# Kernel tuning notes

Hardware: AMD Instinct MI355X
Metric: run time of the kernel (lower is better)

Reference implementation:

```python
import jax, jax.numpy as jnp
import numpy as np
from jax import lax

TOP_K = 200
IOU_THR = 0.5
SCORE_FLOOR = 0.01  # torch code breaks when top score < 0.01

BATCH, N_ANCHOR, N_CLASS_FG = 32, 24564, 80  # last dim of x = 4 + 1 + 80 = 85


def setup_inputs() -> dict:
    key = jax.random.key(0)
    k1, k2 = jax.random.split(key)
    x = jax.random.normal(k1, (BATCH, N_ANCHOR, 4 + 1 + N_CLASS_FG), dtype=jnp.float32)
    # anchors: (cx, cy, w, h) in normalized coords
    anchor = jax.random.uniform(k2, (N_ANCHOR, 4), dtype=jnp.float32, minval=0.05, maxval=0.95)
    return {"x": x, "anchor": anchor}


def _iou_one_vs_all(box1, boxes):
    # box1: [4] (x1,y1,x2,y2); boxes: [N,4] -> ious [N]
    b1x1, b1y1, b1x2, b1y2 = box1[0], box1[1], box1[2], box1[3]
    b2x1, b2y1, b2x2, b2y2 = boxes[:, 0], boxes[:, 1], boxes[:, 2], boxes[:, 3]
    area1 = (b1x2 - b1x1) * (b1y2 - b1y1)
    area2 = (b2x2 - b2x1) * (b2y2 - b2y1)
    xl = jnp.maximum(b1x1, b2x1)
    xr = jnp.minimum(b1x2, b2x2)
    yt = jnp.maximum(b1y1, b2y1)
    yb = jnp.minimum(b1y2, b2y2)
    # torch code clamps intersection extents to [0, 1]
    common = jnp.clip(xr - xl, 0.0, 1.0) * jnp.clip(yb - yt, 0.0, 1.0)
    return common / (area1 + area2 - common)


def _nms_single(cls_i, score_i, box_i):
    # cls_i [N] int, score_i [N], box_i [N,4] -> keep [TOP_K, 6]
    order = jnp.argsort(-score_i)  # descending
    c = cls_i[order].astype(box_i.dtype)
    s = score_i[order]
    b = box_i[order]
    dets = jnp.concatenate([c[:, None], s[:, None], b], axis=1)  # [N, 6]
    valid0 = jnp.ones((dets.shape[0],), dtype=bool)

    def step(valid, _):
        idx = jnp.argmax(valid)  # first still-valid (highest-score) box
        ok = valid[idx] & (s[idx] >= SCORE_FLOOR)
        row = jnp.where(ok, dets[idx], jnp.zeros((6,), dets.dtype))
        ious = _iou_one_vs_all(b[idx], b)  # [N]
        new_valid = valid & (ious < IOU_THR)
        new_valid = new_valid.at[idx].set(False)
        valid = jnp.where(ok, new_valid, valid)
        return valid, row

    _, keep = lax.scan(step, valid0, None, length=TOP_K)
    return keep  # [TOP_K, 6] = (class, score, x1, y1, x2, y2)


def _postprocess(x, anchor):
    # decode boxes
    d = x[:, :, :4]                          # [B, A, 4]
    ax, ay, aw, ah = (anchor[None, :, i] for i in range(4))  # each [1, A]
    cx = d[:, :, 0] * aw / 10.0 + ax
    cy = d[:, :, 1] * ah / 10.0 + ay
    w = jnp.exp(d[:, :, 2] / 5.0) * aw
    h = jnp.exp(d[:, :, 3] / 5.0) * ah
    box = jnp.stack([cx - w / 2.0, cy - h / 2.0, cx + w / 2.0, cy + h / 2.0], axis=2)  # [B,A,4] x1y1x2y2
    # class scores: softmax over (bg + fg), then max over foreground classes
    probs = jax.nn.softmax(x[:, :, 4:], axis=2)
    fg = probs[:, :, 1:]
    score = jnp.max(fg, axis=2)              # [B, A]
    cls = jnp.argmax(fg, axis=2)             # [B, A] foreground class index
    return jax.vmap(_nms_single)(cls, score, box)  # [B, TOP_K, 6]


def reference(x, anchor):
    return _postprocess(x, anchor)
```

## Files before the change

### kernel.cpp

```cpp
#include <hip/hip_runtime.h>
#include <math.h>

#define NB   32
#define NA   24564
#define NTOT (NB * NA)
#define NCH  85
#define TOPK 200
#define IOU_THR_F     0.5f
#define SCORE_FLOOR_F 0.01f

#define DEC_T 128
#define NMS_T 512
#define SLOTS ((NA + NMS_T - 1) / NMS_T)
#define KPASS 8
#define NPOOL (2 * NMS_T)
#define CKADDR(e) ((((e) & 15) << 6) | ((e) >> 4))

__global__ __launch_bounds__(DEC_T) void decode_kernel(
    const float* __restrict__ x, const float* __restrict__ anchor,
    float4* __restrict__ boxes, float* __restrict__ scores,
    float* __restrict__ clsf)
{
    __shared__ float tile[DEC_T * NCH];

    const int base = blockIdx.x * DEC_T;
    const float4* src = (const float4*)(x + (size_t)base * NCH);
    float4* dst = (float4*)tile;
    for (int k = threadIdx.x; k < DEC_T * NCH / 4; k += DEC_T) dst[k] = src[k];
    __syncthreads();

    const int g = base + threadIdx.x;
    const int i = g % NA;
    const float* row = tile + threadIdx.x * NCH;

    float ax = anchor[i * 4 + 0];
    float ay = anchor[i * 4 + 1];
    float aw = anchor[i * 4 + 2];
    float ah = anchor[i * 4 + 3];

    float d0 = row[0], d1 = row[1], d2 = row[2], d3 = row[3];
    float cx = __fadd_rn(__fdiv_rn(__fmul_rn(d0, aw), 10.0f), ax);
    float cy = __fadd_rn(__fdiv_rn(__fmul_rn(d1, ah), 10.0f), ay);
    float w = __fmul_rn((float)exp((double)__fdiv_rn(d2, 5.0f)), aw);
    float h = __fmul_rn((float)exp((double)__fdiv_rn(d3, 5.0f)), ah);
    float hw = __fmul_rn(w, 0.5f);
    float hh = __fmul_rn(h, 0.5f);
    boxes[g] = make_float4(__fsub_rn(cx, hw), __fsub_rn(cy, hh),
                           __fadd_rn(cx, hw), __fadd_rn(cy, hh));

    const float* z = row + 4;
    float m = z[0];
    #pragma unroll 9
    for (int k = 1; k < 81; k++) m = fmaxf(m, z[k]);

    double S = 0.0;
    double be = 0.0;
    float  bz = -INFINITY;
    int    bj = 0;
    for (int k = 0; k < 81; k++) {
        float zk = z[k];
        double e = exp((double)__fsub_rn(zk, m));
        S += e;
        if (k >= 1 && zk > bz) { bz = zk; be = e; bj = k - 1; }
    }
    scores[g] = (float)(be / S);
    clsf[g]   = (float)bj;
}

__device__ __forceinline__ bool suppressed_by(const float4 v, const float a2,
                                              const float4 w, const float a1)
{
    float xl = fmaxf(w.x, v.x);
    float xr = fminf(w.z, v.z);
    float yt = fmaxf(w.y, v.y);
    float yb = fminf(w.w, v.w);
    float cw  = fminf(fmaxf(__fsub_rn(xr, xl), 0.0f), 1.0f);
    float chh = fminf(fmaxf(__fsub_rn(yb, yt), 0.0f), 1.0f);
    float common = __fmul_rn(cw, chh);
    float denom  = __fsub_rn(__fadd_rn(a1, a2), common);
    float iou    = __fdiv_rn(common, denom);
    return !(iou < IOU_THR_F);
}

__global__ __launch_bounds__(NMS_T, 1) void nms_kernel(
    const float4* __restrict__ boxes, const float* __restrict__ scores,
    const float* __restrict__ clsf, float* __restrict__ out)
{
    __shared__ float s_score[NA];
    __shared__ unsigned long long s_ckey[NPOOL];
    __shared__ float4 s_cbox[NPOOL];

    const int b    = blockIdx.x;
    const int tid  = threadIdx.x;
    const int lane = tid & 63;
    const float*  sc = scores + (size_t)b * NA;
    const float4* bx = boxes  + (size_t)b * NA;
    const float*  cf = clsf   + (size_t)b * NA;
    float* ob = out + (size_t)b * TOPK * 6;

    float4 box[SLOTS];
    unsigned long long alive = 0ULL;
    #pragma unroll
    for (int s = 0; s < SLOTS; s++) {
        int j = tid + s * NMS_T;
        box[s] = make_float4(0.0f, 0.0f, 0.0f, 0.0f);
        if (j < NA) { box[s] = bx[j]; alive |= (1ULL << s); }
    }
    for (int j = tid; j < NA; j += NMS_T) s_score[j] = sc[j];

    float4 wbox[KPASS]; float warea[KPASS]; float wscore[KPASS]; int wj[KPASS];
    int t = 0; bool gdone = false; int npass = 0;

    {
        unsigned long long k1 = 0ULL, k2 = 0ULL; int j1 = -1, j2 = -1;
        #pragma unroll
        for (int s = 0; s < SLOTS; s++) {
            if (!(alive & (1ULL << s))) continue;
            int j = tid + s * NMS_T;
            unsigned long long kk =
                ((unsigned long long)__float_as_uint(s_score[j]) << 32) |
                ((unsigned long long)(unsigned)(NA - j) << 10);
            if (kk > k1)      { k2 = k1; j2 = j1; k1 = kk; j1 = j; }
            else if (kk > k2) { k2 = kk; j2 = j; }
        }
        int e0 = 2 * tid, e1 = 2 * tid + 1;
        s_ckey[CKADDR(e0)] = (j1 >= 0) ? (k1 | (unsigned long long)e0) : 1ULL;
        s_ckey[CKADDR(e1)] = (j2 >= 0) ? (k2 | (unsigned long long)e1) : 1ULL;
        if (j1 >= 0) s_cbox[e0] = bx[j1];
        if (j2 >= 0) s_cbox[e1] = bx[j2];
    }
    __syncthreads();

    while (true) {
        unsigned long long ck[16];
        #pragma unroll
        for (int i = 0; i < 16; i++) ck[i] = s_ckey[(i << 6) | lane];

        npass = 0;
        unsigned long long hbound = 0ULL;
        int kmax = TOPK - t; if (kmax > KPASS) kmax = KPASS;
        while (true) {
            unsigned long long lm = 0ULL;
            #pragma unroll
            for (int i = 0; i < 16; i++) if (ck[i] > lm) lm = ck[i];
            #pragma unroll
            for (int off = 32; off > 0; off >>= 1) {
                unsigned long long o = __shfl_xor(lm, off, 64);
                if (o > lm) lm = o;
            }
            if (!(lm > hbound)) break;
            float ms = __uint_as_float((unsigned)(lm >> 32));
            if (!(ms >= SCORE_FLOOR_F)) { gdone = true; break; }

            int e  = (int)(lm & 1023ULL);
            int jw = NA - (int)((lm >> 10) & 0x7FFFULL);
            float4 cb = s_cbox[e];
            float  ca = __fmul_rn(__fsub_rn(cb.z, cb.x), __fsub_rn(cb.w, cb.y));

            bool kill = false;
            #pragma unroll
            for (int k = 0; k < KPASS; k++)
                if (k < npass)
                    kill |= suppressed_by(cb, ca, wbox[k], warea[k]);

            {
                int olane = e >> 4, oi = e & 15;
                unsigned long long pk = 0ULL;
                #pragma unroll
                for (int i = 0; i < 16; i++) if (i == (oi ^ 1)) pk = ck[i];
                unsigned long long hb_c =
                    (lane == olane && pk == 0ULL) ? lm : 0ULL;
                unsigned long long hb = __shfl(hb_c, olane, 64);
                if (hb > hbound) hbound = hb;
                #pragma unroll
                for (int i = 0; i < 16; i++)
                    if (lane == olane && i == oi) ck[i] = 0ULL;
            }

            if (!kill) {
                #pragma unroll
                for (int k = 0; k < KPASS; k++)
                    if (k == npass) {
                        wbox[k] = cb; warea[k] = ca; wscore[k] = ms; wj[k] = jw;
                    }
                npass++;
                if (npass == kmax) break;
            }
        }

        #pragma unroll
        for (int k = 0; k < KPASS; k++) {
            if (k < npass && tid == (wj[k] & (NMS_T - 1))) {
                float* o6 = ob + (size_t)(t + k) * 6;
                o6[0] = cf[wj[k]];
                o6[1] = wscore[k];
                o6[2] = wbox[k].x; o6[3] = wbox[k].y;
                o6[4] = wbox[k].z; o6[5] = wbox[k].w;
            }
        }
        t += npass;
        if (gdone || t >= TOPK) break;

        __syncthreads();

        #pragma unroll
        for (int k = 0; k < KPASS; k++)
            if (k < npass && tid == (wj[k] & (NMS_T - 1)))
                alive &= ~(1ULL << (wj[k] >> 9));

        {
            unsigned long long k1 = 0ULL, k2 = 0ULL; int j1 = -1, j2 = -1;
            #pragma unroll
            for (int s = 0; s < SLOTS; s++) {
                if (!(alive & (1ULL << s))) continue;
                float4 v = box[s];
                float a2 = __fmul_rn(__fsub_rn(v.z, v.x), __fsub_rn(v.w, v.y));
                bool dead = false;
                #pragma unroll
                for (int k = 0; k < KPASS; k++)
                    if (k < npass)
                        dead |= suppressed_by(v, a2, wbox[k], warea[k]);
                if (dead) { alive &= ~(1ULL << s); continue; }
                int j = tid + s * NMS_T;
                unsigned long long kk =
                    ((unsigned long long)__float_as_uint(s_score[j]) << 32) |
                    ((unsigned long long)(unsigned)(NA - j) << 10);
                if (kk > k1)      { k2 = k1; j2 = j1; k1 = kk; j1 = j; }
                else if (kk > k2) { k2 = kk; j2 = j; }
            }
            int e0 = 2 * tid, e1 = 2 * tid + 1;
            s_ckey[CKADDR(e0)] = (j1 >= 0) ? (k1 | (unsigned long long)e0) : 1ULL;
            s_ckey[CKADDR(e1)] = (j2 >= 0) ? (k2 | (unsigned long long)e1) : 1ULL;
            if (j1 >= 0) s_cbox[e0] = bx[j1];
            if (j2 >= 0) s_cbox[e1] = bx[j2];
        }
        __syncthreads();
    }

    for (int k = t * 6 + tid; k < TOPK * 6; k += NMS_T) ob[k] = 0.0f;
}

extern "C" void kernel_launch(void* const* d_in, const int* in_sizes, int n_in,
                              void* d_out, int out_size, void* d_ws, size_t ws_size,
                              hipStream_t stream) {
    const float* x      = (const float*)d_in[0];
    const float* anchor = (const float*)d_in[1];
    float* out = (float*)d_out;

    char* ws = (char*)d_ws;
    const size_t boxes_bytes  = (size_t)NTOT * 16;
    const size_t scores_off   = (boxes_bytes + 255) & ~255ULL;
    const size_t scores_bytes = (size_t)NTOT * 4;
    const size_t cls_off      = (scores_off + scores_bytes + 255) & ~255ULL;

    float4* boxes  = (float4*)ws;
    float*  scores = (float*)(ws + scores_off);
    float*  clsf   = (float*)(ws + cls_off);

    decode_kernel<<<NTOT / DEC_T, DEC_T, 0, stream>>>(x, anchor, boxes, scores, clsf);
    nms_kernel<<<NB, NMS_T, 0, stream>>>(boxes, scores, clsf, out);
}
```

Before: 2.026 ms.

## Split candidate keys to 32-bit, use DPP wave max, move winners to LDS

Replaces the 64-bit packed candidate keys with separate 32-bit score and low-key arrays. The wave-wide max is now two 32-bit DPP reductions plus readlane instead of 64-bit shuffle-xor loops. The per-pass winner boxes move from per-thread register arrays into shared memory, and the suppression sweep is restructured into a winner-outer loop. This cuts shuffle cost and register pressure, but adds LDS reads and a second reduction per selection step.

```diff
diff --git a/kernel.cpp b/kernel.cpp
--- a/kernel.cpp
+++ b/kernel.cpp
@@ -82,13 +82,34 @@
     return !(iou < IOU_THR_F);
 }
 
+__device__ __forceinline__ unsigned wave_umax_dpp(unsigned v)
+{
+    int x = (int)v;
+    #define DPP_ST(C) { \
+        int y_ = __builtin_amdgcn_update_dpp(x, x, C, 0xF, 0xF, false); \
+        x = ((unsigned)y_ > (unsigned)x) ? y_ : x; }
+    DPP_ST(0x111)
+    DPP_ST(0x112)
+    DPP_ST(0x114)
+    DPP_ST(0x118)
+    DPP_ST(0x142)
+    DPP_ST(0x143)
+    #undef DPP_ST
+    return (unsigned)__builtin_amdgcn_readlane(x, 63);
+}
+
 __global__ __launch_bounds__(NMS_T, 1) void nms_kernel(
     const float4* __restrict__ boxes, const float* __restrict__ scores,
     const float* __restrict__ clsf, float* __restrict__ out)
 {
     __shared__ float s_score[NA];
-    __shared__ unsigned long long s_ckey[NPOOL];
+    __shared__ unsigned s_cs[NPOOL];
+    __shared__ unsigned s_cl[NPOOL];
     __shared__ float4 s_cbox[NPOOL];
+    __shared__ float4 s_pwbox[KPASS];
+    __shared__ float  s_pwarea[KPASS];
+    __shared__ float  s_pwscore[KPASS];
+    __shared__ int    s_pwj[KPASS];
 
     const int b    = blockIdx.x;
     const int tid  = threadIdx.x;
@@ -108,8 +129,7 @@
     }
     for (int j = tid; j < NA; j += NMS_T) s_score[j] = sc[j];
 
-    float4 wbox[KPASS]; float warea[KPASS]; float wscore[KPASS]; int wj[KPASS];
-    int t = 0; bool gdone = false; int npass = 0;
+    int t = 0; bool gdone = false;
 
     {
         unsigned long long k1 = 0ULL, k2 = 0ULL; int j1 = -1, j2 = -1;
@@ -124,78 +144,83 @@
             else if (kk > k2) { k2 = kk; j2 = j; }
         }
         int e0 = 2 * tid, e1 = 2 * tid + 1;
-        s_ckey[CKADDR(e0)] = (j1 >= 0) ? (k1 | (unsigned long long)e0) : 1ULL;
-        s_ckey[CKADDR(e1)] = (j2 >= 0) ? (k2 | (unsigned long long)e1) : 1ULL;
+        s_cs[CKADDR(e0)] = (j1 >= 0) ? (unsigned)(k1 >> 32) : 1u;
+        s_cl[CKADDR(e0)] = (unsigned)k1 | (unsigned)e0;
+        s_cs[CKADDR(e1)] = (j2 >= 0) ? (unsigned)(k2 >> 32) : 1u;
+        s_cl[CKADDR(e1)] = (unsigned)k2 | (unsigned)e1;
         if (j1 >= 0) s_cbox[e0] = bx[j1];
         if (j2 >= 0) s_cbox[e1] = bx[j2];
     }
     __syncthreads();
 
     while (true) {
-        unsigned long long ck[16];
+        unsigned cs[16], cl[16];
         #pragma unroll
-        for (int i = 0; i < 16; i++) ck[i] = s_ckey[(i << 6) | lane];
-
-        npass = 0;
+        for (int i = 0; i < 16; i++) {
+            cs[i] = s_cs[(i << 6) | lane];
+            cl[i] = s_cl[(i << 6) | lane];
+        }
+
+        int npass = 0;
         unsigned long long hbound = 0ULL;
         int kmax = TOPK - t; if (kmax > KPASS) kmax = KPASS;
         while (true) {
-            unsigned long long lm = 0ULL;
-            #pragma unroll
-            for (int i = 0; i < 16; i++) if (ck[i] > lm) lm = ck[i];
-            #pragma unroll
-            for (int off = 32; off > 0; off >>= 1) {
-                unsigned long long o = __shfl_xor(lm, off, 64);
-                if (o > lm) lm = o;
-            }
+            unsigned msl = 0u;
+            #pragma unroll
+            for (int i = 0; i < 16; i++) msl = (cs[i] > msl) ? cs[i] : msl;
+            unsigned ms = wave_umax_dpp(msl);
+            unsigned lol = 0u;
+            #pragma unroll
+            for (int i = 0; i < 16; i++)
+                if (cs[i] == ms) lol = (cl[i] > lol) ? cl[i] : lol;
+            unsigned lo = wave_umax_dpp(lol);
+            unsigned long long lm = ((unsigned long long)ms << 32) | lo;
+
             if (!(lm > hbound)) break;
-            float ms = __uint_as_float((unsigned)(lm >> 32));
-            if (!(ms >= SCORE_FLOOR_F)) { gdone = true; break; }
-
-            int e  = (int)(lm & 1023ULL);
-            int jw = NA - (int)((lm >> 10) & 0x7FFFULL);
+            float msf = __uint_as_float(ms);
+            if (!(msf >= SCORE_FLOOR_F)) { gdone = true; break; }
+
+            int e  = (int)(lo & 1023u);
+            int jw = NA - (int)((lo >> 10) & 0x7FFFu);
             float4 cb = s_cbox[e];
             float  ca = __fmul_rn(__fsub_rn(cb.z, cb.x), __fsub_rn(cb.w, cb.y));
 
             bool kill = false;
-            #pragma unroll
-            for (int k = 0; k < KPASS; k++)
-                if (k < npass)
-                    kill |= suppressed_by(cb, ca, wbox[k], warea[k]);
-
-            {
-                int olane = e >> 4, oi = e & 15;
-                unsigned long long pk = 0ULL;
-                #pragma unroll
-                for (int i = 0; i < 16; i++) if (i == (oi ^ 1)) pk = ck[i];
-                unsigned long long hb_c =
-                    (lane == olane && pk == 0ULL) ? lm : 0ULL;
-                unsigned long long hb = __shfl(hb_c, olane, 64);
-                if (hb > hbound) hbound = hb;
-                #pragma unroll
-                for (int i = 0; i < 16; i++)
-                    if (lane == olane && i == oi) ck[i] = 0ULL;
-            }
+            for (int k = 0; k < npass; k++) {
+                float4 wb = s_pwbox[k];
+                kill |= suppressed_by(cb, ca, wb, s_pwarea[k]);
+            }
+
+            int olane = e >> 4, oi = e & 15;
+            unsigned pks = 0u;
+            #pragma unroll
+            for (int i = 0; i < 16; i++) if (i == (oi ^ 1)) pks = cs[i];
+            unsigned pkol = (unsigned)__builtin_amdgcn_readlane((int)pks, olane);
+            if (pkol == 0u) hbound = lm;
+            bool me = (lane == olane);
+            #pragma unroll
+            for (int i = 0; i < 16; i++) if (i == oi && me) cs[i] = 0u;
 
             if (!kill) {
-                #pragma unroll
-                for (int k = 0; k < KPASS; k++)
-                    if (k == npass) {
-                        wbox[k] = cb; warea[k] = ca; wscore[k] = ms; wj[k] = jw;
-                    }
+                if (lane == 0) {
+                    s_pwbox[npass]   = cb;
+                    s_pwarea[npass]  = ca;
+                    s_pwscore[npass] = msf;
+                    s_pwj[npass]     = jw;
+                }
                 npass++;
                 if (npass == kmax) break;
             }
         }
 
-        #pragma unroll
-        for (int k = 0; k < KPASS; k++) {
-            if (k < npass && tid == (wj[k] & (NMS_T - 1))) {
+        for (int k = 0; k < npass; k++) {
+            int jw = s_pwj[k];
+            if (tid == (jw & (NMS_T - 1))) {
+                float4 wb = s_pwbox[k];
                 float* o6 = ob + (size_t)(t + k) * 6;
-                o6[0] = cf[wj[k]];
-                o6[1] = wscore[k];
-                o6[2] = wbox[k].x; o6[3] = wbox[k].y;
-                o6[4] = wbox[k].z; o6[5] = wbox[k].w;
+                o6[0] = cf[jw];
+                o6[1] = s_pwscore[k];
+                o6[2] = wb.x; o6[3] = wb.y; o6[4] = wb.z; o6[5] = wb.w;
             }
         }
         t += npass;
@@ -203,24 +228,28 @@
 
         __syncthreads();
 
-        #pragma unroll
-        for (int k = 0; k < KPASS; k++)
-            if (k < npass && tid == (wj[k] & (NMS_T - 1)))
-                alive &= ~(1ULL << (wj[k] >> 9));
-
+        for (int k = 0; k < npass; k++) {
+            int jw = s_pwj[k];
+            if (tid == (jw & (NMS_T - 1))) alive &= ~(1ULL << (jw >> 9));
+        }
+        for (int k = 0; k < npass; k++) {
+            float4 wb = s_pwbox[k];
+            float  wa = s_pwarea[k];
+            #pragma unroll
+            for (int s = 0; s < SLOTS; s++) {
+                if (alive & (1ULL << s)) {
+                    float4 v = box[s];
+                    float a2 = __fmul_rn(__fsub_rn(v.z, v.x),
+                                         __fsub_rn(v.w, v.y));
+                    if (suppressed_by(v, a2, wb, wa)) alive &= ~(1ULL << s);
+                }
+            }
+        }
         {
             unsigned long long k1 = 0ULL, k2 = 0ULL; int j1 = -1, j2 = -1;
             #pragma unroll
             for (int s = 0; s < SLOTS; s++) {
                 if (!(alive & (1ULL << s))) continue;
-                float4 v = box[s];
-                float a2 = __fmul_rn(__fsub_rn(v.z, v.x), __fsub_rn(v.w, v.y));
-                bool dead = false;
-                #pragma unroll
-                for (int k = 0; k < KPASS; k++)
-                    if (k < npass)
-                        dead |= suppressed_by(v, a2, wbox[k], warea[k]);
-                if (dead) { alive &= ~(1ULL << s); continue; }
                 int j = tid + s * NMS_T;
                 unsigned long long kk =
                     ((unsigned long long)__float_as_uint(s_score[j]) << 32) |
@@ -229,8 +258,10 @@
                 else if (kk > k2) { k2 = kk; j2 = j; }
             }
             int e0 = 2 * tid, e1 = 2 * tid + 1;
-            s_ckey[CKADDR(e0)] = (j1 >= 0) ? (k1 | (unsigned long long)e0) : 1ULL;
-            s_ckey[CKADDR(e1)] = (j2 >= 0) ? (k2 | (unsigned long long)e1) : 1ULL;
+            s_cs[CKADDR(e0)] = (j1 >= 0) ? (unsigned)(k1 >> 32) : 1u;
+            s_cl[CKADDR(e0)] = (unsigned)k1 | (unsigned)e0;
+            s_cs[CKADDR(e1)] = (j2 >= 0) ? (unsigned)(k2 >> 32) : 1u;
+            s_cl[CKADDR(e1)] = (unsigned)k2 | (unsigned)e1;
             if (j1 >= 0) s_cbox[e0] = bx[j1];
             if (j2 >= 0) s_cbox[e1] = bx[j2];
         }
```

New measurement: 2.299 ms. +13.4%, slower.
